# Performance work log

Measured on AMD Instinct MI355X. Metric: run time of the kernel, lower is better.

Reference implementation:

```python
import jax, jax.numpy as jnp
import numpy as np

N = 50000
E = 800000
EP = 200000
IN_C = 128
HID = 128


def setup_inputs() -> dict:
    key = jax.random.key(0)
    ks = jax.random.split(key, 10)
    x = jax.random.normal(ks[0], (N, IN_C), dtype=jnp.float32)
    edge_index = jax.random.randint(ks[1], (2, E), 0, N, dtype=jnp.int64)
    pred_edges = jax.random.randint(ks[2], (2, EP), 0, N, dtype=jnp.int64)
    s_in = 1.0 / np.sqrt(IN_C)
    s_h = 1.0 / np.sqrt(HID)
    W1l = jax.random.normal(ks[3], (IN_C, HID), dtype=jnp.float32) * s_in
    W1r = jax.random.normal(ks[4], (IN_C, HID), dtype=jnp.float32) * s_in
    b1 = jnp.zeros((HID,), dtype=jnp.float32)
    W2l = jax.random.normal(ks[5], (HID, HID), dtype=jnp.float32) * s_h
    W2r = jax.random.normal(ks[6], (HID, HID), dtype=jnp.float32) * s_h
    b2 = jnp.zeros((HID,), dtype=jnp.float32)
    return {"x": x, "W1l": W1l, "b1": b1, "W1r": W1r,
            "W2l": W2l, "b2": b2, "W2r": W2r,
            "edge_index": edge_index, "pred_edges": pred_edges}


def _sage_conv(h, Wl, b, Wr, src, dst, n_nodes):
    # PyG SAGEConv (aggr='mean'): out = lin_l(mean_j x_j) + lin_r(x_i)
    msg = h[src]                                              # (E, D) gather
    agg = jax.ops.segment_sum(msg, dst, num_segments=n_nodes)  # (N, D) scatter-add
    deg = jax.ops.segment_sum(jnp.ones((src.shape[0],), h.dtype), dst,
                              num_segments=n_nodes)
    agg = agg / jnp.maximum(deg, 1.0)[:, None]                # mean (0 for isolated)
    return agg @ Wl + b + h @ Wr


def reference(x, W1l, b1, W1r, W2l, b2, W2r, edge_index, pred_edges):
    n_nodes = x.shape[0]
    src, dst = edge_index[0], edge_index[1]
    h = jax.nn.relu(_sage_conv(x, W1l, b1, W1r, src, dst, n_nodes))
    z = _sage_conv(h, W2l, b2, W2r, src, dst, n_nodes)
    ps, pd = pred_edges[0], pred_edges[1]
    return jnp.sum(z[ps] * z[pd], axis=-1)  # (E_pred,) logits
```

## Files before the change

### kernel.cpp

```cpp
#include <hip/hip_runtime.h>

#define D 128

typedef __attribute__((ext_vector_type(8))) short short8;
typedef __attribute__((ext_vector_type(4))) float f32x4;

__device__ inline unsigned int f2bf_bits(float f) {
    unsigned int u = __float_as_uint(f);
    return (u + 0x7FFFu + ((u >> 16) & 1u)) >> 16;
}

__device__ inline float bfhi(unsigned int u) { return __uint_as_float(u << 16); }
__device__ inline float bflo(unsigned int u) { return __uint_as_float(u & 0xffff0000u); }

__global__ __launch_bounds__(256) void prep_kernel(
    const float* __restrict__ x,
    const float* __restrict__ W1l, const float* __restrict__ W1r,
    const float* __restrict__ W2l, const float* __restrict__ W2r,
    unsigned short* __restrict__ xbf, unsigned short* __restrict__ xlo,
    unsigned short* __restrict__ h1, unsigned short* __restrict__ l1,
    unsigned short* __restrict__ h2, unsigned short* __restrict__ l2,
    int n4, int ncast, int* __restrict__ chist, int* __restrict__ csrpad)
{
    const int b = blockIdx.x;
    const int t = threadIdx.x;
    if (b < ncast) {
        int i = b * 256 + t;
        if (i >= n4) return;
        f32x4 v = *(const f32x4*)(x + (size_t)i * 4);
        ushort4 oh, ol;
        {
            unsigned int h; float hf;
            h = f2bf_bits(v.x); hf = __uint_as_float(h << 16);
            oh.x = (unsigned short)h; ol.x = (unsigned short)f2bf_bits(v.x - hf);
            h = f2bf_bits(v.y); hf = __uint_as_float(h << 16);
            oh.y = (unsigned short)h; ol.y = (unsigned short)f2bf_bits(v.y - hf);
            h = f2bf_bits(v.z); hf = __uint_as_float(h << 16);
            oh.z = (unsigned short)h; ol.z = (unsigned short)f2bf_bits(v.z - hf);
            h = f2bf_bits(v.w); hf = __uint_as_float(h << 16);
            oh.w = (unsigned short)h; ol.w = (unsigned short)f2bf_bits(v.w - hf);
        }
        *(ushort4*)(xbf + (size_t)i * 4) = oh;
        *(ushort4*)(xlo + (size_t)i * 4) = ol;
    } else if (b < ncast + 256) {
        int gidx = (b - ncast) * 256 + t;
        int sel = gidx >> 15;
        int idx = gidx & 32767;
        int tt = idx >> 12;
        int ks = (idx >> 9) & 7;
        int lane = (idx >> 3) & 63;
        int j = idx & 7;
        int qq = lane >> 4, r16 = lane & 15;
        int k = ks * 32 + qq * 8 + j;
        int c = tt * 16 + r16;
        const float* Wl = sel ? W2l : W1l;
        const float* Wr = sel ? W2r : W1r;
        float v = (k < 128) ? Wl[k * 128 + c] : Wr[(k - 128) * 128 + c];
        unsigned int h = f2bf_bits(v);
        float hf = __uint_as_float(h << 16);
        unsigned int l = f2bf_bits(v - hf);
        (sel ? h2 : h1)[idx] = (unsigned short)h;
        (sel ? l2 : l1)[idx] = (unsigned short)l;
    } else {
        chist[t] = 0;
        if (t < 16) csrpad[t] = 0;
    }
}

__global__ __launch_bounds__(256) void coarse_count_kernel(const int* __restrict__ dst,
                                                           int* __restrict__ chist, int E) {
    __shared__ int h[256];
    h[threadIdx.x] = 0;
    __syncthreads();
    const int stride = gridDim.x * 256;
    for (int e = blockIdx.x * 256 + threadIdx.x; e < E; e += stride)
        atomicAdd(&h[dst[e] >> 8], 1);
    __syncthreads();
    int v = h[threadIdx.x];
    if (v) atomicAdd(&chist[threadIdx.x], v);
}

__global__ __launch_bounds__(256) void scan256_kernel(const int* __restrict__ chist,
                                                      int* __restrict__ cbase,
                                                      int* __restrict__ gcur) {
    __shared__ int wsum[4];
    const int t = threadIdx.x, lane = t & 63, wv = t >> 6;
    int v = chist[t];
    int s = v;
#pragma unroll
    for (int o = 1; o < 64; o <<= 1) {
        int u = __shfl_up(s, o, 64);
        if (lane >= o) s += u;
    }
    if (lane == 63) wsum[wv] = s;
    __syncthreads();
    int add = 0;
    for (int w = 0; w < wv; ++w) add += wsum[w];
    cbase[t + 1] = s + add;
    if (t == 0) cbase[0] = 0;
    gcur[t] = s + add - v;
}

#define CCHUNK 4096
__global__ __launch_bounds__(256) void coarse_scatter_kernel(
    const int* __restrict__ src, const int* __restrict__ dst,
    int* __restrict__ gcur, unsigned int* __restrict__ centries, int E)
{
    __shared__ int h[256];
    __shared__ int base[256];
    __shared__ unsigned int stage[CCHUNK];
    const int t = threadIdx.x;
    const int e0 = blockIdx.x * CCHUNK;
    h[t] = 0;
    __syncthreads();
#pragma unroll
    for (int i = 0; i < 16; ++i) {
        int e = e0 + i * 256 + t;
        unsigned int u = 0xFFFFFFFFu;
        if (e < E) {
            int d = dst[e];
            int s = src[e];
            int b = d >> 8;
            u = ((unsigned)b << 24) | ((unsigned)s << 8) | (unsigned)(d & 255);
            atomicAdd(&h[b], 1);
        }
        stage[i * 256 + t] = u;
    }
    __syncthreads();
    base[t] = atomicAdd(&gcur[t], h[t]);
    __syncthreads();
    h[t] = 0;
    __syncthreads();
#pragma unroll
    for (int i = 0; i < 16; ++i) {
        unsigned int u = stage[i * 256 + t];
        if (u != 0xFFFFFFFFu) {
            int b = u >> 24;
            int r = atomicAdd(&h[b], 1);
            centries[base[b] + r] = u & 0x00FFFFFFu;
        }
    }
}

#define DCAP 8192
__global__ __launch_bounds__(256) void fine_bucket_kernel(
    const unsigned int* __restrict__ centries,
    const int* __restrict__ cbase,
    int* __restrict__ offo, int* __restrict__ csr, int N, int E)
{
    __shared__ int h[256], ex[256], wsum[4];
    __shared__ int stg[DCAP];
    const int t = threadIdx.x, lane = t & 63, wv = t >> 6;
    const int b = blockIdx.x;
    const int s0 = cbase[b];
    const int cnt = cbase[b + 1] - s0;
    h[t] = 0;
    __syncthreads();
    for (int i = t; i < cnt; i += 256)
        atomicAdd(&h[centries[s0 + i] & 255], 1);
    __syncthreads();
    int v = h[t], s = v;
#pragma unroll
    for (int o = 1; o < 64; o <<= 1) {
        int u = __shfl_up(s, o, 64);
        if (lane >= o) s += u;
    }
    if (lane == 63) wsum[wv] = s;
    __syncthreads();
    int add = 0;
    for (int w = 0; w < wv; ++w) add += wsum[w];
    const int exc = s + add - v;
    ex[t] = exc;
    const int dg = b * 256 + t;
    if (dg < N) offo[dg] = s0 + exc;
    if (b == 0 && t == 0) offo[N] = E;
    h[t] = 0;
    __syncthreads();
    if (cnt <= DCAP) {
        for (int i = t; i < cnt; i += 256) {
            unsigned int u = centries[s0 + i];
            int dl = u & 255;
            int r = atomicAdd(&h[dl], 1);
            stg[ex[dl] + r] = (int)(u >> 8);
        }
        __syncthreads();
        for (int i = t; i < cnt; i += 256)
            csr[s0 + i] = stg[i];
    } else {
        for (int i = t; i < cnt; i += 256) {
            unsigned int u = centries[s0 + i];
            int dl = u & 255;
            int r = atomicAdd(&h[dl], 1);
            csr[s0 + ex[dl] + r] = (int)(u >> 8);
        }
    }
}

__global__ __launch_bounds__(256, 4) void fused_sage_kernel(
    const unsigned short* __restrict__ featbf,
    const int* __restrict__ off,
    const int* __restrict__ csr,
    const unsigned short* __restrict__ self_hi,
    const unsigned short* __restrict__ self_lo,
    const unsigned short* __restrict__ wpk_hi,
    const unsigned short* __restrict__ wpk_lo,
    const float* __restrict__ bias,
    unsigned short* __restrict__ out_hi,
    unsigned short* __restrict__ out_lo,
    int do_relu)
{
    __shared__ unsigned short AHs[4][64][8];
    __shared__ unsigned short ALs[4][64][8];
    __shared__ unsigned short outs_hi[16][128];
    __shared__ unsigned short outs_lo[16][128];

    const int w = threadIdx.x >> 6;
    const int l = threadIdx.x & 63;
    const int tile = blockIdx.x;
    const int n0w = tile * 16;

    const int gn = l >> 2;
    const int q2 = l & 3;
    const int gnode = n0w + gn;
    const int start = off[gnode];
    const int end   = off[gnode + 1];
    const unsigned short* fb = featbf + w * 32 + q2 * 8;

    float ga[8] = {0.f, 0.f, 0.f, 0.f, 0.f, 0.f, 0.f, 0.f};

#define ACC(rv)                                                         \
    { ga[0] += bfhi(rv.x); ga[1] += bflo(rv.x);                         \
      ga[2] += bfhi(rv.y); ga[3] += bflo(rv.y);                         \
      ga[4] += bfhi(rv.z); ga[5] += bflo(rv.z);                         \
      ga[6] += bfhi(rv.w); ga[7] += bflo(rv.w); }

    const uint4 zero4 = {0u, 0u, 0u, 0u};
    if (start < end) {
        int4 ix = *(const int4*)(csr + start);
        uint4 c0 = *(const uint4*)(fb + (size_t)ix.x * D);
        uint4 c1 = *(const uint4*)(fb + (size_t)ix.y * D);
        uint4 c2 = *(const uint4*)(fb + (size_t)ix.z * D);
        uint4 c3 = *(const uint4*)(fb + (size_t)ix.w * D);
        for (int e = start; e < end; e += 4) {
            int4 ixn = *(const int4*)(csr + e + 4);
            uint4 n0 = *(const uint4*)(fb + (size_t)ixn.x * D);
            uint4 n1 = *(const uint4*)(fb + (size_t)ixn.y * D);
            uint4 n2 = *(const uint4*)(fb + (size_t)ixn.z * D);
            uint4 n3 = *(const uint4*)(fb + (size_t)ixn.w * D);
            if (e + 1 >= end) c1 = zero4;
            if (e + 2 >= end) c2 = zero4;
            if (e + 3 >= end) c3 = zero4;
            ACC(c0) ACC(c1) ACC(c2) ACC(c3)
            c0 = n0; c1 = n1; c2 = n2; c3 = n3;
        }
    }
#undef ACC

    {
        const float dinv = 1.0f / (float)max(end - start, 1);
        short8 hi8, lo8;
#pragma unroll
        for (int c = 0; c < 8; ++c) {
            float v = ga[c] * dinv;
            unsigned int hb = f2bf_bits(v);
            hi8[c] = (short)hb;
            lo8[c] = (short)f2bf_bits(v - __uint_as_float(hb << 16));
        }
        *(short8*)&AHs[w][q2 * 16 + gn][0] = hi8;
        *(short8*)&ALs[w][q2 * 16 + gn][0] = lo8;
    }
    __syncthreads();

    const int q = l >> 4, r16 = l & 15;
    const int mnode = n0w + r16;
    f32x4 acc0 = {0.f, 0.f, 0.f, 0.f};
    f32x4 acc1 = {0.f, 0.f, 0.f, 0.f};
    const unsigned short* sph = self_hi + (size_t)mnode * D + q * 8;
    const unsigned short* spl = self_lo + (size_t)mnode * D + q * 8;
    const unsigned short* bh0 = wpk_hi + (size_t)(2 * w) * 4096 + l * 8;
    const unsigned short* bl0 = wpk_lo + (size_t)(2 * w) * 4096 + l * 8;

#pragma unroll
    for (int ks = 0; ks < 8; ++ks) {
        short8 AH, AL;
        if (ks < 4) {
            AH = *(const short8*)&AHs[ks][l][0];
            AL = *(const short8*)&ALs[ks][l][0];
        } else {
            AH = *(const short8*)(sph + (ks - 4) * 32);
            AL = *(const short8*)(spl + (ks - 4) * 32);
        }
        short8 BH0 = *(const short8*)(bh0 + ks * 512);
        short8 BL0 = *(const short8*)(bl0 + ks * 512);
        short8 BH1 = *(const short8*)(bh0 + 4096 + ks * 512);
        short8 BL1 = *(const short8*)(bl0 + 4096 + ks * 512);
        acc0 = __builtin_amdgcn_mfma_f32_16x16x32_bf16(AH, BH0, acc0, 0, 0, 0);
        acc0 = __builtin_amdgcn_mfma_f32_16x16x32_bf16(AL, BH0, acc0, 0, 0, 0);
        acc0 = __builtin_amdgcn_mfma_f32_16x16x32_bf16(AH, BL0, acc0, 0, 0, 0);
        acc1 = __builtin_amdgcn_mfma_f32_16x16x32_bf16(AH, BH1, acc1, 0, 0, 0);
        acc1 = __builtin_amdgcn_mfma_f32_16x16x32_bf16(AL, BH1, acc1, 0, 0, 0);
        acc1 = __builtin_amdgcn_mfma_f32_16x16x32_bf16(AH, BL1, acc1, 0, 0, 0);
    }

    {
        const float bv0 = bias[32 * w + r16];
        const float bv1 = bias[32 * w + 16 + r16];
#pragma unroll
        for (int r = 0; r < 4; ++r) {
            float v0 = acc0[r] + bv0;
            float v1 = acc1[r] + bv1;
            if (do_relu) { v0 = fmaxf(v0, 0.f); v1 = fmaxf(v1, 0.f); }
            const int row = q * 4 + r;
            unsigned int h0 = f2bf_bits(v0);
            unsigned int h1 = f2bf_bits(v1);
            outs_hi[row][32 * w + r16] = (unsigned short)h0;
            outs_hi[row][32 * w + 16 + r16] = (unsigned short)h1;
            outs_lo[row][32 * w + r16] =
                (unsigned short)f2bf_bits(v0 - __uint_as_float(h0 << 16));
            outs_lo[row][32 * w + 16 + r16] =
                (unsigned short)f2bf_bits(v1 - __uint_as_float(h1 << 16));
        }
    }
    __syncthreads();
    {
        const int tid = threadIdx.x;
        short8 vh = *(short8*)(&outs_hi[0][0] + tid * 8);
        *(short8*)(out_hi + (size_t)n0w * D + tid * 8) = vh;
        if (out_lo) {
            short8 vl = *(short8*)(&outs_lo[0][0] + tid * 8);
            *(short8*)(out_lo + (size_t)n0w * D + tid * 8) = vl;
        }
    }
}

__global__ __launch_bounds__(256) void pred_kernel(const unsigned short* __restrict__ zbf,
                                                   const int* __restrict__ ps,
                                                   const int* __restrict__ pd,
                                                   float* __restrict__ out, int EP) {
    int idx = blockIdx.x * blockDim.x + threadIdx.x;
    int e = idx >> 5;
    if (e >= EP) return;
    int l = idx & 31;
    const unsigned short* fb = zbf + (size_t)l * 4;
    uint2 ra = *(const uint2*)(fb + (size_t)ps[e] * D);
    uint2 rb = *(const uint2*)(fb + (size_t)pd[e] * D);
    float p = __uint_as_float(ra.x << 16)         * __uint_as_float(rb.x << 16)
            + __uint_as_float(ra.x & 0xffff0000u) * __uint_as_float(rb.x & 0xffff0000u)
            + __uint_as_float(ra.y << 16)         * __uint_as_float(rb.y << 16)
            + __uint_as_float(ra.y & 0xffff0000u) * __uint_as_float(rb.y & 0xffff0000u);
#pragma unroll
    for (int off = 16; off > 0; off >>= 1) p += __shfl_xor(p, off, 32);
    if (l == 0) out[e] = p;
}

extern "C" void kernel_launch(void* const* d_in, const int* in_sizes, int n_in,
                              void* d_out, int out_size, void* d_ws, size_t ws_size,
                              hipStream_t stream) {
    const float* x   = (const float*)d_in[0];
    const float* W1l = (const float*)d_in[1];
    const float* b1  = (const float*)d_in[2];
    const float* W1r = (const float*)d_in[3];
    const float* W2l = (const float*)d_in[4];
    const float* b2  = (const float*)d_in[5];
    const float* W2r = (const float*)d_in[6];
    const int* edge_index = (const int*)d_in[7];
    const int* pred_edges = (const int*)d_in[8];
    float* out = (float*)d_out;

    const int N  = in_sizes[0] / D;
    const int E  = in_sizes[7] / 2;
    const int EP = in_sizes[8] / 2;

    const int* src = edge_index;
    const int* dst = edge_index + E;
    const int* ps  = pred_edges;
    const int* pd  = pred_edges + EP;

    int* chist   = (int*)d_ws;
    int* cbase   = chist + 256;
    int* gcur    = cbase + 272;
    int* off     = gcur + 256;
    unsigned int* centries = (unsigned int*)(off + 50016);
    int* csr     = (int*)(centries + E);
    unsigned short* w1_hi = (unsigned short*)(csr + E + 16);
    unsigned short* w1_lo = w1_hi + 32768;
    unsigned short* w2_hi = w1_lo + 32768;
    unsigned short* w2_lo = w2_hi + 32768;
    unsigned short* xbf   = w2_lo + 32768;
    unsigned short* xlo   = xbf + (size_t)N * D;
    unsigned short* hbf   = xlo + (size_t)N * D;
    unsigned short* hlo   = hbf + (size_t)N * D;
    unsigned short* zbf   = hlo + (size_t)N * D;

    const int n4 = N * D / 4;
    const int ncast = (n4 + 255) / 256;
    const int ntiles = N / 16;
    const int nbC = (E + CCHUNK - 1) / CCHUNK;
    const int nbD = (N + 255) / 256;
    const int nblk_pred = (EP * 32 + 255) / 256;

    prep_kernel<<<ncast + 257, 256, 0, stream>>>(x, W1l, W1r, W2l, W2r,
                                                 xbf, xlo, w1_hi, w1_lo, w2_hi, w2_lo,
                                                 n4, ncast, chist, csr + E);

    coarse_count_kernel<<<256, 256, 0, stream>>>(dst, chist, E);
    scan256_kernel<<<1, 256, 0, stream>>>(chist, cbase, gcur);
    coarse_scatter_kernel<<<nbC, 256, 0, stream>>>(src, dst, gcur, centries, E);
    fine_bucket_kernel<<<nbD, 256, 0, stream>>>(centries, cbase, off, csr, N, E);

    fused_sage_kernel<<<ntiles, 256, 0, stream>>>(xbf, off, csr, xbf, xlo,
                                                  w1_hi, w1_lo, b1, hbf, hlo, 1);
    fused_sage_kernel<<<ntiles, 256, 0, stream>>>(hbf, off, csr, hbf, hlo,
                                                  w2_hi, w2_lo, b2, zbf,
                                                  (unsigned short*)nullptr, 0);
    pred_kernel<<<nblk_pred, 256, 0, stream>>>(zbf, ps, pd, out, EP);
}
```

Baseline: 247.3 us.

## Split fused SAGE into sliced gather and GEMM kernels with column-sliced feature layout

Result: slower. 258.6 us (+4.6%).

```diff
diff --git a/kernel.cpp b/kernel.cpp
--- a/kernel.cpp
+++ b/kernel.cpp
@@ -17,10 +17,10 @@
     const float* __restrict__ x,
     const float* __restrict__ W1l, const float* __restrict__ W1r,
     const float* __restrict__ W2l, const float* __restrict__ W2r,
-    unsigned short* __restrict__ xbf, unsigned short* __restrict__ xlo,
+    unsigned short* __restrict__ xsl_hi, unsigned short* __restrict__ xsl_lo,
     unsigned short* __restrict__ h1, unsigned short* __restrict__ l1,
     unsigned short* __restrict__ h2, unsigned short* __restrict__ l2,
-    int n4, int ncast, int* __restrict__ chist, int* __restrict__ csrpad)
+    int n4, int ncast, int N, int* __restrict__ chist, int* __restrict__ csrpad)
 {
     const int b = blockIdx.x;
     const int t = threadIdx.x;
@@ -40,8 +40,11 @@
             h = f2bf_bits(v.w); hf = __uint_as_float(h << 16);
             oh.w = (unsigned short)h; ol.w = (unsigned short)f2bf_bits(v.w - hf);
         }
-        *(ushort4*)(xbf + (size_t)i * 4) = oh;
-        *(ushort4*)(xlo + (size_t)i * 4) = ol;
+        int node = i >> 5;
+        int c0 = (i & 31) * 4;
+        size_t o = (size_t)(c0 >> 5) * N * 32 + (size_t)node * 32 + (c0 & 31);
+        *(ushort4*)(xsl_hi + o) = oh;
+        *(ushort4*)(xsl_lo + o) = ol;
     } else if (b < ncast + 256) {
         int gidx = (b - ncast) * 256 + t;
         int sel = gidx >> 15;
@@ -63,7 +66,7 @@
         (sel ? l2 : l1)[idx] = (unsigned short)l;
     } else {
         chist[t] = 0;
-        if (t < 16) csrpad[t] = 0;
+        if (t < 32) csrpad[t] = 0;
     }
 }
 
@@ -196,35 +199,25 @@
     }
 }
 
-__global__ __launch_bounds__(256, 4) void fused_sage_kernel(
-    const unsigned short* __restrict__ featbf,
+__global__ __launch_bounds__(256) void gather_slice_kernel(
+    const unsigned short* __restrict__ featsl,
     const int* __restrict__ off,
     const int* __restrict__ csr,
-    const unsigned short* __restrict__ self_hi,
-    const unsigned short* __restrict__ self_lo,
-    const unsigned short* __restrict__ wpk_hi,
-    const unsigned short* __restrict__ wpk_lo,
-    const float* __restrict__ bias,
-    unsigned short* __restrict__ out_hi,
-    unsigned short* __restrict__ out_lo,
-    int do_relu)
+    unsigned short* __restrict__ agg_hi,
+    unsigned short* __restrict__ agg_lo,
+    int N, int ntiles)
 {
-    __shared__ unsigned short AHs[4][64][8];
-    __shared__ unsigned short ALs[4][64][8];
-    __shared__ unsigned short outs_hi[16][128];
-    __shared__ unsigned short outs_lo[16][128];
-
-    const int w = threadIdx.x >> 6;
-    const int l = threadIdx.x & 63;
-    const int tile = blockIdx.x;
-    const int n0w = tile * 16;
-
-    const int gn = l >> 2;
-    const int q2 = l & 3;
-    const int gnode = n0w + gn;
-    const int start = off[gnode];
-    const int end   = off[gnode + 1];
-    const unsigned short* fb = featbf + w * 32 + q2 * 8;
+    const int bid = blockIdx.x;
+    const int s = (bid & 7) >> 1;
+    const int k = ((bid >> 3) << 1) | (bid & 1);
+    const int w = threadIdx.x >> 6, l = threadIdx.x & 63;
+    const int t16 = k * 4 + w;
+    if (t16 >= ntiles) return;
+    const int gn = l >> 2, q2 = l & 3;
+    const int node = t16 * 16 + gn;
+    const int start = off[node];
+    const int end   = off[node + 1];
+    const unsigned short* fb = featsl + (size_t)s * N * 32 + q2 * 8;
 
     float ga[8] = {0.f, 0.f, 0.f, 0.f, 0.f, 0.f, 0.f, 0.f};
 
@@ -237,16 +230,16 @@
     const uint4 zero4 = {0u, 0u, 0u, 0u};
     if (start < end) {
         int4 ix = *(const int4*)(csr + start);
-        uint4 c0 = *(const uint4*)(fb + (size_t)ix.x * D);
-        uint4 c1 = *(const uint4*)(fb + (size_t)ix.y * D);
-        uint4 c2 = *(const uint4*)(fb + (size_t)ix.z * D);
-        uint4 c3 = *(const uint4*)(fb + (size_t)ix.w * D);
+        uint4 c0 = *(const uint4*)(fb + (size_t)ix.x * 32);
+        uint4 c1 = *(const uint4*)(fb + (size_t)ix.y * 32);
+        uint4 c2 = *(const uint4*)(fb + (size_t)ix.z * 32);
+        uint4 c3 = *(const uint4*)(fb + (size_t)ix.w * 32);
         for (int e = start; e < end; e += 4) {
             int4 ixn = *(const int4*)(csr + e + 4);
-            uint4 n0 = *(const uint4*)(fb + (size_t)ixn.x * D);
-            uint4 n1 = *(const uint4*)(fb + (size_t)ixn.y * D);
-            uint4 n2 = *(const uint4*)(fb + (size_t)ixn.z * D);
-            uint4 n3 = *(const uint4*)(fb + (size_t)ixn.w * D);
+            uint4 n0 = *(const uint4*)(fb + (size_t)ixn.x * 32);
+            uint4 n1 = *(const uint4*)(fb + (size_t)ixn.y * 32);
+            uint4 n2 = *(const uint4*)(fb + (size_t)ixn.z * 32);
+            uint4 n3 = *(const uint4*)(fb + (size_t)ixn.w * 32);
             if (e + 1 >= end) c1 = zero4;
             if (e + 2 >= end) c2 = zero4;
             if (e + 3 >= end) c3 = zero4;
@@ -256,27 +249,46 @@
     }
 #undef ACC
 
-    {
-        const float dinv = 1.0f / (float)max(end - start, 1);
-        short8 hi8, lo8;
-#pragma unroll
-        for (int c = 0; c < 8; ++c) {
-            float v = ga[c] * dinv;
-            unsigned int hb = f2bf_bits(v);
-            hi8[c] = (short)hb;
-            lo8[c] = (short)f2bf_bits(v - __uint_as_float(hb << 16));
-        }
-        *(short8*)&AHs[w][q2 * 16 + gn][0] = hi8;
-        *(short8*)&ALs[w][q2 * 16 + gn][0] = lo8;
-    }
-    __syncthreads();
-
+    const float dinv = 1.0f / (float)max(end - start, 1);
+    short8 hi8, lo8;
+#pragma unroll
+    for (int c = 0; c < 8; ++c) {
+        float v = ga[c] * dinv;
+        unsigned int hb = f2bf_bits(v);
+        hi8[c] = (short)hb;
+        lo8[c] = (short)f2bf_bits(v - __uint_as_float(hb << 16));
+    }
+    const size_t p = ((size_t)(t16 * 4 + s) * 64 + q2 * 16 + gn) * 8;
+    *(short8*)(agg_hi + p) = hi8;
+    *(short8*)(agg_lo + p) = lo8;
+}
+
+__global__ __launch_bounds__(256, 4) void sage_gemm_kernel(
+    const unsigned short* __restrict__ agg_hi,
+    const unsigned short* __restrict__ agg_lo,
+    const unsigned short* __restrict__ selfsl_hi,
+    const unsigned short* __restrict__ selfsl_lo,
+    const unsigned short* __restrict__ wpk_hi,
+    const unsigned short* __restrict__ wpk_lo,
+    const float* __restrict__ bias,
+    unsigned short* __restrict__ outsl_hi,
+    unsigned short* __restrict__ outsl_lo,
+    int N, int do_relu)
+{
+    __shared__ unsigned short outs_hi[16][128];
+    __shared__ unsigned short outs_lo[16][128];
+
+    const int w = threadIdx.x >> 6;
+    const int l = threadIdx.x & 63;
+    const int tile = blockIdx.x;
+    const int n0w = tile * 16;
     const int q = l >> 4, r16 = l & 15;
     const int mnode = n0w + r16;
+
     f32x4 acc0 = {0.f, 0.f, 0.f, 0.f};
     f32x4 acc1 = {0.f, 0.f, 0.f, 0.f};
-    const unsigned short* sph = self_hi + (size_t)mnode * D + q * 8;
-    const unsigned short* spl = self_lo + (size_t)mnode * D + q * 8;
+    const unsigned short* aph = agg_hi + (size_t)tile * 2048 + l * 8;
+    const unsigned short* apl = agg_lo + (size_t)tile * 2048 + l * 8;
     const unsigned short* bh0 = wpk_hi + (size_t)(2 * w) * 4096 + l * 8;
     const unsigned short* bl0 = wpk_lo + (size_t)(2 * w) * 4096 + l * 8;
 
@@ -284,11 +296,12 @@
     for (int ks = 0; ks < 8; ++ks) {
         short8 AH, AL;
         if (ks < 4) {
-            AH = *(const short8*)&AHs[ks][l][0];
-            AL = *(const short8*)&ALs[ks][l][0];
+            AH = *(const short8*)(aph + ks * 512);
+            AL = *(const short8*)(apl + ks * 512);
         } else {
-            AH = *(const short8*)(sph + (ks - 4) * 32);
-            AL = *(const short8*)(spl + (ks - 4) * 32);
+            const size_t so = (size_t)(ks - 4) * N * 32 + (size_t)mnode * 32 + q * 8;
+            AH = *(const short8*)(selfsl_hi + so);
+            AL = *(const short8*)(selfsl_lo + so);
         }
         short8 BH0 = *(const short8*)(bh0 + ks * 512);
         short8 BL0 = *(const short8*)(bl0 + ks * 512);
@@ -324,33 +337,36 @@
     __syncthreads();
     {
         const int tid = threadIdx.x;
-        short8 vh = *(short8*)(&outs_hi[0][0] + tid * 8);
-        *(short8*)(out_hi + (size_t)n0w * D + tid * 8) = vh;
-        if (out_lo) {
-            short8 vl = *(short8*)(&outs_lo[0][0] + tid * 8);
-            *(short8*)(out_lo + (size_t)n0w * D + tid * 8) = vl;
-        }
-    }
-}
-
-__global__ __launch_bounds__(256) void pred_kernel(const unsigned short* __restrict__ zbf,
+        const int row = tid >> 4, ch8 = tid & 15;
+        const size_t o = (size_t)(ch8 >> 2) * N * 32
+                       + (size_t)(n0w + row) * 32 + (ch8 & 3) * 8;
+        short8 vh = *(short8*)(&outs_hi[row][ch8 * 8]);
+        *(short8*)(outsl_hi + o) = vh;
+        if (outsl_lo) {
+            short8 vl = *(short8*)(&outs_lo[row][ch8 * 8]);
+            *(short8*)(outsl_lo + o) = vl;
+        }
+    }
+}
+
+__global__ __launch_bounds__(256) void pred_kernel(const unsigned short* __restrict__ zsl,
                                                    const int* __restrict__ ps,
                                                    const int* __restrict__ pd,
-                                                   float* __restrict__ out, int EP) {
-    int idx = blockIdx.x * blockDim.x + threadIdx.x;
-    int e = idx >> 5;
+                                                   float* __restrict__ out, int N, int EP) {
+    int idx = blockIdx.x * 256 + threadIdx.x;
+    int e = idx >> 4;
     if (e >= EP) return;
-    int l = idx & 31;
-    const unsigned short* fb = zbf + (size_t)l * 4;
-    uint2 ra = *(const uint2*)(fb + (size_t)ps[e] * D);
-    uint2 rb = *(const uint2*)(fb + (size_t)pd[e] * D);
-    float p = __uint_as_float(ra.x << 16)         * __uint_as_float(rb.x << 16)
-            + __uint_as_float(ra.x & 0xffff0000u) * __uint_as_float(rb.x & 0xffff0000u)
-            + __uint_as_float(ra.y << 16)         * __uint_as_float(rb.y << 16)
-            + __uint_as_float(ra.y & 0xffff0000u) * __uint_as_float(rb.y & 0xffff0000u);
-#pragma unroll
-    for (int off = 16; off > 0; off >>= 1) p += __shfl_xor(p, off, 32);
-    if (l == 0) out[e] = p;
+    int L = idx & 15;
+    const unsigned short* fb = zsl + (size_t)(L >> 2) * N * 32 + (L & 3) * 8;
+    uint4 ra = *(const uint4*)(fb + (size_t)ps[e] * 32);
+    uint4 rb = *(const uint4*)(fb + (size_t)pd[e] * 32);
+    float p = bfhi(ra.x) * bfhi(rb.x) + bflo(ra.x) * bflo(rb.x)
+            + bfhi(ra.y) * bfhi(rb.y) + bflo(ra.y) * bflo(rb.y)
+            + bfhi(ra.z) * bfhi(rb.z) + bflo(ra.z) * bflo(rb.z)
+            + bfhi(ra.w) * bfhi(rb.w) + bflo(ra.w) * bflo(rb.w);
+#pragma unroll
+    for (int off = 8; off > 0; off >>= 1) p += __shfl_xor(p, off, 16);
+    if (L == 0) out[e] = p;
 }
 
 extern "C" void kernel_launch(void* const* d_in, const int* in_sizes, int n_in,
@@ -382,36 +398,43 @@
     int* off     = gcur + 256;
     unsigned int* centries = (unsigned int*)(off + 50016);
     int* csr     = (int*)(centries + E);
-    unsigned short* w1_hi = (unsigned short*)(csr + E + 16);
+    unsigned short* w1_hi = (unsigned short*)(csr + E + 32);
     unsigned short* w1_lo = w1_hi + 32768;
     unsigned short* w2_hi = w1_lo + 32768;
     unsigned short* w2_lo = w2_hi + 32768;
-    unsigned short* xbf   = w2_lo + 32768;
-    unsigned short* xlo   = xbf + (size_t)N * D;
-    unsigned short* hbf   = xlo + (size_t)N * D;
-    unsigned short* hlo   = hbf + (size_t)N * D;
-    unsigned short* zbf   = hlo + (size_t)N * D;
+    unsigned short* xsl_hi = w2_lo + 32768;
+    unsigned short* xsl_lo = xsl_hi + (size_t)N * D;
+    unsigned short* hsl_hi = xsl_lo + (size_t)N * D;
+    unsigned short* hsl_lo = hsl_hi + (size_t)N * D;
+    unsigned short* zsl    = hsl_lo + (size_t)N * D;
+    unsigned short* agg_hi = zsl + (size_t)N * D;
+    unsigned short* agg_lo = agg_hi + (size_t)N * D;
 
     const int n4 = N * D / 4;
     const int ncast = (n4 + 255) / 256;
     const int ntiles = N / 16;
+    const int nblk_gather = ((ntiles + 3) / 4) * 4;
     const int nbC = (E + CCHUNK - 1) / CCHUNK;
     const int nbD = (N + 255) / 256;
-    const int nblk_pred = (EP * 32 + 255) / 256;
+    const int nblk_pred = (EP * 16 + 255) / 256;
 
     prep_kernel<<<ncast + 257, 256, 0, stream>>>(x, W1l, W1r, W2l, W2r,
-                                                 xbf, xlo, w1_hi, w1_lo, w2_hi, w2_lo,
-                                                 n4, ncast, chist, csr + E);
+                                                 xsl_hi, xsl_lo, w1_hi, w1_lo, w2_hi, w2_lo,
+                                                 n4, ncast, N, chist, csr + E);
 
     coarse_count_kernel<<<256, 256, 0, stream>>>(dst, chist, E);
     scan256_kernel<<<1, 256, 0, stream>>>(chist, cbase, gcur);
     coarse_scatter_kernel<<<nbC, 256, 0, stream>>>(src, dst, gcur, centries, E);
     fine_bucket_kernel<<<nbD, 256, 0, stream>>>(centries, cbase, off, csr, N, E);
 
-    fused_sage_kernel<<<ntiles, 256, 0, stream>>>(xbf, off, csr, xbf, xlo,
-                                                  w1_hi, w1_lo, b1, hbf, hlo, 1);
-    fused_sage_kernel<<<ntiles, 256, 0, stream>>>(hbf, off, csr, hbf, hlo,
-                                                  w2_hi, w2_lo, b2, zbf,
-                                                  (unsigned short*)nullptr, 0);
-    pred_kernel<<<nblk_pred, 256, 0, stream>>>(zbf, ps, pd, out, EP);
-}
+    gather_slice_kernel<<<nblk_gather, 256, 0, stream>>>(xsl_hi, off, csr,
+                                                         agg_hi, agg_lo, N, ntiles);
+    sage_gemm_kernel<<<ntiles, 256, 0, stream>>>(agg_hi, agg_lo, xsl_hi, xsl_lo,
+                                                 w1_hi, w1_lo, b1, hsl_hi, hsl_lo, N, 1);
+    gather_slice_kernel<<<nblk_gather, 256, 0, stream>>>(hsl_hi, off, csr,
+                                                         agg_hi, agg_lo, N, ntiles);
+    sage_gemm_kernel<<<ntiles, 256, 0, stream>>>(agg_hi, agg_lo, hsl_hi, hsl_lo,
+                                                 w2_hi, w2_lo, b2, zsl,
+                                                 (unsigned short*)nullptr, N, 0);
+    pred_kernel<<<nblk_pred, 256, 0, stream>>>(zsl, ps, pd, out, N, EP);
+}
```

## Fuse coarse dst histogram into prep kernel and widen pred-kernel loads

Applied to the files above, without the earlier changes.

After: 255.4 us. 3.3% more time.

```diff
diff --git a/kernel.cpp b/kernel.cpp
--- a/kernel.cpp
+++ b/kernel.cpp
@@ -17,11 +17,13 @@
     const float* __restrict__ x,
     const float* __restrict__ W1l, const float* __restrict__ W1r,
     const float* __restrict__ W2l, const float* __restrict__ W2r,
+    const int* __restrict__ dst, int E,
     unsigned short* __restrict__ xbf, unsigned short* __restrict__ xlo,
     unsigned short* __restrict__ h1, unsigned short* __restrict__ l1,
     unsigned short* __restrict__ h2, unsigned short* __restrict__ l2,
-    int n4, int ncast, int* __restrict__ chist, int* __restrict__ csrpad)
+    int n4, int ncast, int* __restrict__ chist2, int* __restrict__ csrpad)
 {
+    __shared__ int h[256];
     const int b = blockIdx.x;
     const int t = threadIdx.x;
     if (b < ncast) {
@@ -30,15 +32,15 @@
         f32x4 v = *(const f32x4*)(x + (size_t)i * 4);
         ushort4 oh, ol;
         {
-            unsigned int h; float hf;
-            h = f2bf_bits(v.x); hf = __uint_as_float(h << 16);
-            oh.x = (unsigned short)h; ol.x = (unsigned short)f2bf_bits(v.x - hf);
-            h = f2bf_bits(v.y); hf = __uint_as_float(h << 16);
-            oh.y = (unsigned short)h; ol.y = (unsigned short)f2bf_bits(v.y - hf);
-            h = f2bf_bits(v.z); hf = __uint_as_float(h << 16);
-            oh.z = (unsigned short)h; ol.z = (unsigned short)f2bf_bits(v.z - hf);
-            h = f2bf_bits(v.w); hf = __uint_as_float(h << 16);
-            oh.w = (unsigned short)h; ol.w = (unsigned short)f2bf_bits(v.w - hf);
+            unsigned int hb; float hf;
+            hb = f2bf_bits(v.x); hf = __uint_as_float(hb << 16);
+            oh.x = (unsigned short)hb; ol.x = (unsigned short)f2bf_bits(v.x - hf);
+            hb = f2bf_bits(v.y); hf = __uint_as_float(hb << 16);
+            oh.y = (unsigned short)hb; ol.y = (unsigned short)f2bf_bits(v.y - hf);
+            hb = f2bf_bits(v.z); hf = __uint_as_float(hb << 16);
+            oh.z = (unsigned short)hb; ol.z = (unsigned short)f2bf_bits(v.z - hf);
+            hb = f2bf_bits(v.w); hf = __uint_as_float(hb << 16);
+            oh.w = (unsigned short)hb; ol.w = (unsigned short)f2bf_bits(v.w - hf);
         }
         *(ushort4*)(xbf + (size_t)i * 4) = oh;
         *(ushort4*)(xlo + (size_t)i * 4) = ol;
@@ -56,36 +58,32 @@
         const float* Wl = sel ? W2l : W1l;
         const float* Wr = sel ? W2r : W1r;
         float v = (k < 128) ? Wl[k * 128 + c] : Wr[(k - 128) * 128 + c];
-        unsigned int h = f2bf_bits(v);
-        float hf = __uint_as_float(h << 16);
+        unsigned int hb = f2bf_bits(v);
+        float hf = __uint_as_float(hb << 16);
         unsigned int l = f2bf_bits(v - hf);
-        (sel ? h2 : h1)[idx] = (unsigned short)h;
+        (sel ? h2 : h1)[idx] = (unsigned short)hb;
         (sel ? l2 : l1)[idx] = (unsigned short)l;
+    } else if (b < ncast + 512) {
+        const int cb = b - ncast - 256;
+        h[t] = 0;
+        __syncthreads();
+        for (int e = cb * 256 + t; e < E; e += 65536)
+            atomicAdd(&h[dst[e] >> 8], 1);
+        __syncthreads();
+        chist2[cb * 256 + t] = h[t];
     } else {
-        chist[t] = 0;
-        if (t < 16) csrpad[t] = 0;
-    }
-}
-
-__global__ __launch_bounds__(256) void coarse_count_kernel(const int* __restrict__ dst,
-                                                           int* __restrict__ chist, int E) {
-    __shared__ int h[256];
-    h[threadIdx.x] = 0;
-    __syncthreads();
-    const int stride = gridDim.x * 256;
-    for (int e = blockIdx.x * 256 + threadIdx.x; e < E; e += stride)
-        atomicAdd(&h[dst[e] >> 8], 1);
-    __syncthreads();
-    int v = h[threadIdx.x];
-    if (v) atomicAdd(&chist[threadIdx.x], v);
-}
-
-__global__ __launch_bounds__(256) void scan256_kernel(const int* __restrict__ chist,
+        if (t < 32) csrpad[t] = 0;
+    }
+}
+
+__global__ __launch_bounds__(256) void scan256_kernel(const int* __restrict__ chist2,
                                                       int* __restrict__ cbase,
                                                       int* __restrict__ gcur) {
     __shared__ int wsum[4];
     const int t = threadIdx.x, lane = t & 63, wv = t >> 6;
-    int v = chist[t];
+    int v = 0;
+#pragma unroll 8
+    for (int b = 0; b < 256; ++b) v += chist2[b * 256 + t];
     int s = v;
 #pragma unroll
     for (int o = 1; o < 64; o <<= 1) {
@@ -337,20 +335,20 @@
                                                    const int* __restrict__ ps,
                                                    const int* __restrict__ pd,
                                                    float* __restrict__ out, int EP) {
-    int idx = blockIdx.x * blockDim.x + threadIdx.x;
-    int e = idx >> 5;
+    int idx = blockIdx.x * 256 + threadIdx.x;
+    int e = idx >> 4;
     if (e >= EP) return;
-    int l = idx & 31;
-    const unsigned short* fb = zbf + (size_t)l * 4;
-    uint2 ra = *(const uint2*)(fb + (size_t)ps[e] * D);
-    uint2 rb = *(const uint2*)(fb + (size_t)pd[e] * D);
-    float p = __uint_as_float(ra.x << 16)         * __uint_as_float(rb.x << 16)
-            + __uint_as_float(ra.x & 0xffff0000u) * __uint_as_float(rb.x & 0xffff0000u)
-            + __uint_as_float(ra.y << 16)         * __uint_as_float(rb.y << 16)
-            + __uint_as_float(ra.y & 0xffff0000u) * __uint_as_float(rb.y & 0xffff0000u);
-#pragma unroll
-    for (int off = 16; off > 0; off >>= 1) p += __shfl_xor(p, off, 32);
-    if (l == 0) out[e] = p;
+    int L = idx & 15;
+    const unsigned short* fb = zbf + (size_t)L * 8;
+    uint4 ra = *(const uint4*)(fb + (size_t)ps[e] * D);
+    uint4 rb = *(const uint4*)(fb + (size_t)pd[e] * D);
+    float p = bfhi(ra.x) * bfhi(rb.x) + bflo(ra.x) * bflo(rb.x)
+            + bfhi(ra.y) * bfhi(rb.y) + bflo(ra.y) * bflo(rb.y)
+            + bfhi(ra.z) * bfhi(rb.z) + bflo(ra.z) * bflo(rb.z)
+            + bfhi(ra.w) * bfhi(rb.w) + bflo(ra.w) * bflo(rb.w);
+#pragma unroll
+    for (int off = 8; off > 0; off >>= 1) p += __shfl_xor(p, off, 16);
+    if (L == 0) out[e] = p;
 }
 
 extern "C" void kernel_launch(void* const* d_in, const int* in_sizes, int n_in,
@@ -376,13 +374,13 @@
     const int* ps  = pred_edges;
     const int* pd  = pred_edges + EP;
 
-    int* chist   = (int*)d_ws;
-    int* cbase   = chist + 256;
+    int* chist2  = (int*)d_ws;
+    int* cbase   = chist2 + 65536;
     int* gcur    = cbase + 272;
     int* off     = gcur + 256;
     unsigned int* centries = (unsigned int*)(off + 50016);
     int* csr     = (int*)(centries + E);
-    unsigned short* w1_hi = (unsigned short*)(csr + E + 16);
+    unsigned short* w1_hi = (unsigned short*)(csr + E + 32);
     unsigned short* w1_lo = w1_hi + 32768;
     unsigned short* w2_hi = w1_lo + 32768;
     unsigned short* w2_lo = w2_hi + 32768;
@@ -397,14 +395,13 @@
     const int ntiles = N / 16;
     const int nbC = (E + CCHUNK - 1) / CCHUNK;
     const int nbD = (N + 255) / 256;
-    const int nblk_pred = (EP * 32 + 255) / 256;
-
-    prep_kernel<<<ncast + 257, 256, 0, stream>>>(x, W1l, W1r, W2l, W2r,
+    const int nblk_pred = (EP * 16 + 255) / 256;
+
+    prep_kernel<<<ncast + 513, 256, 0, stream>>>(x, W1l, W1r, W2l, W2r, dst, E,
                                                  xbf, xlo, w1_hi, w1_lo, w2_hi, w2_lo,
-                                                 n4, ncast, chist, csr + E);
-
-    coarse_count_kernel<<<256, 256, 0, stream>>>(dst, chist, E);
-    scan256_kernel<<<1, 256, 0, stream>>>(chist, cbase, gcur);
+                                                 n4, ncast, chist2, csr + E);
+
+    scan256_kernel<<<1, 256, 0, stream>>>(chist2, cbase, gcur);
     coarse_scatter_kernel<<<nbC, 256, 0, stream>>>(src, dst, gcur, centries, E);
     fine_bucket_kernel<<<nbD, 256, 0, stream>>>(centries, cbase, off, csr, N, E);
 
```
